# Kernel optimization log

Measured on AMD Instinct MI355X. Metric: run time of the kernel, lower is better.

Reference implementation:

```python
import jax, jax.numpy as jnp
import numpy as np

B, S, H, D = 2, 2048, 16, 64


def setup_inputs() -> dict:
    key = jax.random.key(0)
    kq, kk, kv, km = jax.random.split(key, 4)
    q = jax.random.normal(kq, (B, S, H, D), dtype=jnp.float32)
    k = jax.random.normal(kk, (B, S, H, D), dtype=jnp.float32)
    v = jax.random.normal(kv, (B, S, H, D), dtype=jnp.float32)
    pattern_mask = jax.random.bernoulli(km, 0.1, (S, S))
    return {"q": q, "k": k, "v": v, "pattern_mask": pattern_mask}


def reference(q, k, v, pattern_mask):
    # Faithful math of the torch module: for each query row i, attend only to
    # columns j where pattern_mask[i, j]; softmax over the selected columns
    # per (batch, head); rows with no selected columns produce zeros.
    head_dim = q.shape[-1]
    scale = 1.0 / jnp.sqrt(jnp.asarray(head_dim, dtype=q.dtype))
    # scores: [B, H, S_q, S_k]
    scores = jnp.einsum('bihd,bjhd->bhij', q, k) * scale
    neg = jnp.finfo(scores.dtype).min
    masked = jnp.where(pattern_mask[None, None, :, :], scores, neg)
    attn = jax.nn.softmax(masked, axis=-1)
    # zero out rows with no active columns (softmax over all-masked row is uniform garbage)
    row_has = jnp.any(pattern_mask, axis=-1)  # [S]
    attn = jnp.where(row_has[None, None, :, None], attn, jnp.zeros((), dtype=attn.dtype))
    # output: [B, S, H, D]
    out = jnp.einsum('bhij,bjhd->bihd', attn, v)
    return out
```

## Files before the change

kernel.cpp:

```cpp
#include <hip/hip_runtime.h>
#include <hip/hip_bf16.h>
#include <math.h>

#define SLEN 2048
#define NBATCH 2
#define NH 16
#define DH 64
#define WPR 64
#define NROUND 32
#define IMGB 8192
#define CONVBLK (NBATCH * NH * NROUND)
#define PACKBLK (SLEN * WPR / 256)

typedef __attribute__((ext_vector_type(4))) short short4v;
typedef __attribute__((ext_vector_type(8))) short short8v;
typedef __attribute__((ext_vector_type(4))) float float4v;
typedef __attribute__((ext_vector_type(16))) float float16v;

typedef __attribute__((address_space(1))) void gas_void;
typedef __attribute__((address_space(3))) void las_void;

__device__ __forceinline__ unsigned short f2bf(float f) {
  unsigned u = __float_as_uint(f);
  u += 0x7fffu + ((u >> 16) & 1u);
  return (unsigned short)(u >> 16);
}

__device__ __forceinline__ float fexp2(float x) {
#if __has_builtin(__builtin_amdgcn_exp2f)
  return __builtin_amdgcn_exp2f(x);
#else
  return __expf(x * 0.6931471805599453f);
#endif
}

__device__ __forceinline__ unsigned pack_bf2(float a, float b) {
  unsigned ua = __float_as_uint(a); ua += 0x7fffu + ((ua >> 16) & 1u);
  unsigned ub = __float_as_uint(b); ub += 0x7fffu + ((ub >> 16) & 1u);
  return __builtin_amdgcn_perm(ub, ua, 0x07060302u);
}

__device__ __forceinline__ unsigned cvtpk(float lo, float hi) {
  unsigned r;
  asm("v_cvt_pk_bf16_f32 %0, %1, %2" : "=v"(r) : "v"(lo), "v"(hi));
  return r;
}

__device__ __forceinline__ unsigned nib4(unsigned w) {
  return ((w * 0x01020408u) >> 24) & 0xFu;
}

__device__ __forceinline__ int vcol(int p) {
  const int kc = 2 * (p >> 5) + ((p >> 4) & 1);
  return 16 * kc + 8 * ((p >> 2) & 1) + 4 * ((p >> 3) & 1) + (p & 3);
}

__global__ __launch_bounds__(256) void prep_kernel(
    const float* __restrict__ kk, const float* __restrict__ vv,
    const void* __restrict__ mask,
    char* __restrict__ kb, char* __restrict__ vb,
    unsigned* __restrict__ packed) {
  const int tid = threadIdx.x;
  if (blockIdx.x >= CONVBLK) {
    const int w = (blockIdx.x - CONVBLK) * 256 + tid;
    const uint4* bp = (const uint4*)((const char*)mask + (size_t)w * 32);
    uint4 x = bp[0], y = bp[1];
    const unsigned orw = (x.x | x.y) | (x.z | x.w) | (y.x | y.y) | (y.z | y.w);
    __shared__ int s0, sm;
    if (tid == 0) { s0 = 0; sm = 0; }
    __syncthreads();
    const int lane0 = ((tid & 63) == 0);
    if (__any((orw & 0x000000ffu) != 0) && lane0) atomicOr(&s0, 1);
    if (__any((orw & 0xffffff00u) != 0) && lane0) atomicOr(&sm, 1);
    __syncthreads();
    unsigned bits;
    if (s0 && sm) {
      bits = nib4(x.x) | (nib4(x.y) << 4) | (nib4(x.z) << 8) | (nib4(x.w) << 12) |
             (nib4(y.x) << 16) | (nib4(y.y) << 20) | (nib4(y.z) << 24) | (nib4(y.w) << 28);
    } else {
      const unsigned* m = (const unsigned*)mask + (size_t)w * 32;
      bits = 0u;
#pragma unroll
      for (int j = 0; j < 32; j++) bits |= (m[j] ? 1u : 0u) << j;
    }
    packed[w] = bits;
    return;
  }
  const int bid = blockIdx.x;
  const int t = bid & 31;
  const int bh = bid >> 5;
  const int b = bh >> 4, h = bh & 15;
  char* kimg = kb + (size_t)bid * IMGB;
  char* vimg = vb + (size_t)bid * IMGB;

  {
    const int r = tid >> 2;
    const int dg = (tid & 3) << 4;
    const float* src = kk + (((size_t)(b * SLEN + t * 64 + r) * NH + h) * DH + dg);
    char* rowp = kimg + r * 128;
    const int swzk = (r & 7) << 4;
#pragma unroll
    for (int i = 0; i < 4; i++) {
      float4v x = *(const float4v*)(src + i * 4);
      const int d0 = dg + i * 4;
      const int off = (d0 * 2) ^ swzk;
      union { unsigned u[2]; short4v s4; } cv;
      cv.u[0] = pack_bf2(x.x, x.y);
      cv.u[1] = pack_bf2(x.z, x.w);
      *(short4v*)(rowp + off) = cv.s4;
    }
  }
  {
    const int d = tid >> 2;
    const int kg = (tid & 3) << 4;
    char* rowp = vimg + d * 128;
    const int swzv = (d & 7) << 4;
    const float* src = vv + ((size_t)(b * SLEN + t * 64 + kg) * NH + h) * DH + d;
#pragma unroll
    for (int i = 0; i < 16; i++) {
      const int p = kg + i;
      float x = src[(size_t)i * (NH * DH)];
      const int off = (vcol(p) * 2) ^ swzv;
      *(unsigned short*)(rowp + off) = f2bf(x);
    }
  }
}

__global__ __launch_bounds__(256, 2) void sattn_fast7(
    const float* __restrict__ q, const unsigned* __restrict__ pmask,
    const char* __restrict__ kb, const char* __restrict__ vb,
    float* __restrict__ out) {
  __shared__ __align__(16) char Kbuf[2][IMGB];
  __shared__ __align__(16) char Vbuf[2][IMGB];

  const int tid = threadIdx.x;
  const int xcd = blockIdx.x & 7;
  const int j = blockIdx.x >> 3;
  const int bh = xcd * 4 + (j >> 4);
  const int chunk = j & 15;
  const int b = bh >> 4;
  const int hd = bh & 15;
  const int wave = tid >> 6;
  const int lane = tid & 63;
  const int l31 = lane & 31;
  const int hl = lane >> 5;
  const int swz = (l31 & 7) << 4;

  const int qrow = chunk * 128 + wave * 32 + l31;
  const int qw = qrow * WPR;

  const float SCL2 = 0.18033688011112042f;
  short8v qf[4];
  {
    const float* qp = q + (((size_t)b * SLEN + qrow) * NH + hd) * DH;
#pragma unroll
    for (int ds = 0; ds < 4; ds++) {
      float4v x0 = *(const float4v*)(qp + ds * 16 + hl * 8);
      float4v x1 = *(const float4v*)(qp + ds * 16 + hl * 8 + 4);
      union { unsigned u[4]; short8v s8; } cv;
      cv.u[0] = pack_bf2(x0.x * SCL2, x0.y * SCL2);
      cv.u[1] = pack_bf2(x0.z * SCL2, x0.w * SCL2);
      cv.u[2] = pack_bf2(x1.x * SCL2, x1.y * SCL2);
      cv.u[3] = pack_bf2(x1.z * SCL2, x1.w * SCL2);
      qf[ds] = cv.s8;
    }
  }

  short8v ones;
#pragma unroll
  for (int i = 0; i < 8; i++) ones[i] = (short)0x3F80;

  const char* gK = kb + (size_t)bh * (NROUND * IMGB) + tid * 16;
  const char* gV = vb + (size_t)bh * (NROUND * IMGB) + tid * 16;

  float16v acc0 = {}, acc1 = {}, lacc = {};

  uint2 m = *(const uint2*)&pmask[qw];

  {
    char* lK = &Kbuf[0][0] + tid * 16;
    char* lV = &Vbuf[0][0] + tid * 16;
#pragma unroll
    for (int i = 0; i < 2; i++) {
      __builtin_amdgcn_global_load_lds((gas_void*)(gK + i * 4096), (las_void*)(lK + i * 4096), 16, 0, 0);
      __builtin_amdgcn_global_load_lds((gas_void*)(gV + i * 4096), (las_void*)(lV + i * 4096), 16, 0, 0);
    }
  }
  __syncthreads();

  for (int t = 0; t < NROUND; t++) {
    const int bt = t & 1;
    const unsigned m0 = m.x, m1 = m.y;
    if (t + 1 < NROUND) {
      m = *(const uint2*)&pmask[qw + 2 * (t + 1)];
      const char* nK = gK + (size_t)(t + 1) * IMGB;
      const char* nV = gV + (size_t)(t + 1) * IMGB;
      char* lK = &Kbuf[bt ^ 1][0] + tid * 16;
      char* lV = &Vbuf[bt ^ 1][0] + tid * 16;
#pragma unroll
      for (int i = 0; i < 2; i++) {
        __builtin_amdgcn_global_load_lds((gas_void*)(nK + i * 4096), (las_void*)(lK + i * 4096), 16, 0, 0);
        __builtin_amdgcn_global_load_lds((gas_void*)(nV + i * 4096), (las_void*)(lV + i * 4096), 16, 0, 0);
      }
    }

    const char* Kl = &Kbuf[bt][0];
    float16v st0, st1;
    __builtin_amdgcn_s_setprio(1);
    {
      float16v z = {};
#pragma unroll
      for (int ds = 0; ds < 4; ds++) {
        short8v kf = *(const short8v*)(Kl + (l31)*128 + ((ds * 32 + hl * 16) ^ swz));
        z = __builtin_amdgcn_mfma_f32_32x32x16_bf16(kf, qf[ds], z, 0, 0, 0);
      }
      st0 = z;
    }
    {
      float16v z = {};
#pragma unroll
      for (int ds = 0; ds < 4; ds++) {
        short8v kf = *(const short8v*)(Kl + (32 + l31) * 128 + ((ds * 32 + hl * 16) ^ swz));
        z = __builtin_amdgcn_mfma_f32_32x32x16_bf16(kf, qf[ds], z, 0, 0, 0);
      }
      st1 = z;
    }
    __builtin_amdgcn_s_setprio(0);

    float p0[16], p1[16];
#pragma unroll
    for (int u = 0; u < 4; u++) {
      const unsigned hw0 = m0 >> (8 * u + 4 * hl);
      const unsigned hw1 = m1 >> (8 * u + 4 * hl);
      {
        float a0 = fexp2(st0[4 * u + 0]); a0 = (hw0 & 1u) ? a0 : 0.f;
        float a1 = fexp2(st0[4 * u + 1]); a1 = (hw0 & 2u) ? a1 : 0.f;
        float a2 = fexp2(st0[4 * u + 2]); a2 = (hw0 & 4u) ? a2 : 0.f;
        float a3 = fexp2(st0[4 * u + 3]); a3 = (hw0 & 8u) ? a3 : 0.f;
        p0[4 * u + 0] = a0; p0[4 * u + 1] = a1; p0[4 * u + 2] = a2; p0[4 * u + 3] = a3;
      }
      {
        float a0 = fexp2(st1[4 * u + 0]); a0 = (hw1 & 1u) ? a0 : 0.f;
        float a1 = fexp2(st1[4 * u + 1]); a1 = (hw1 & 2u) ? a1 : 0.f;
        float a2 = fexp2(st1[4 * u + 2]); a2 = (hw1 & 4u) ? a2 : 0.f;
        float a3 = fexp2(st1[4 * u + 3]); a3 = (hw1 & 8u) ? a3 : 0.f;
        p1[4 * u + 0] = a0; p1[4 * u + 1] = a1; p1[4 * u + 2] = a2; p1[4 * u + 3] = a3;
      }
    }
    short8v pf[4];
    {
      union { unsigned u[4]; short8v s8; } c0, c1, c2, c3;
#pragma unroll
      for (int jj = 0; jj < 4; jj++) {
        c0.u[jj] = cvtpk(p0[2 * jj], p0[2 * jj + 1]);
        c1.u[jj] = cvtpk(p0[8 + 2 * jj], p0[8 + 2 * jj + 1]);
        c2.u[jj] = cvtpk(p1[2 * jj], p1[2 * jj + 1]);
        c3.u[jj] = cvtpk(p1[8 + 2 * jj], p1[8 + 2 * jj + 1]);
      }
      pf[0] = c0.s8; pf[1] = c1.s8; pf[2] = c2.s8; pf[3] = c3.s8;
    }

    const char* Vl = &Vbuf[bt][0];
    __builtin_amdgcn_s_setprio(1);
#pragma unroll
    for (int kc = 0; kc < 4; kc++) {
      short8v vf0 = *(const short8v*)(Vl + (l31)*128 + ((kc * 32 + hl * 16) ^ swz));
      acc0 = __builtin_amdgcn_mfma_f32_32x32x16_bf16(vf0, pf[kc], acc0, 0, 0, 0);
      short8v vf1 = *(const short8v*)(Vl + (32 + l31) * 128 + ((kc * 32 + hl * 16) ^ swz));
      acc1 = __builtin_amdgcn_mfma_f32_32x32x16_bf16(vf1, pf[kc], acc1, 0, 0, 0);
      lacc = __builtin_amdgcn_mfma_f32_32x32x16_bf16(ones, pf[kc], lacc, 0, 0, 0);
    }
    __builtin_amdgcn_s_setprio(0);
    __syncthreads();
  }

  const float l = lacc[0];
  const float inv = (l > 0.f) ? 1.f / l : 0.f;
  float* op = out + (((size_t)b * SLEN + qrow) * NH + hd) * DH;
#pragma unroll
  for (int u = 0; u < 4; u++) {
    float4v o0, o1;
    o0.x = acc0[4 * u + 0] * inv; o0.y = acc0[4 * u + 1] * inv;
    o0.z = acc0[4 * u + 2] * inv; o0.w = acc0[4 * u + 3] * inv;
    o1.x = acc1[4 * u + 0] * inv; o1.y = acc1[4 * u + 1] * inv;
    o1.z = acc1[4 * u + 2] * inv; o1.w = acc1[4 * u + 3] * inv;
    *(float4v*)(op + 8 * u + 4 * hl) = o0;
    *(float4v*)(op + 32 + 8 * u + 4 * hl) = o1;
  }
}

__global__ __launch_bounds__(256) void sattn_fallback(
    const float* __restrict__ q, const float* __restrict__ kk,
    const float* __restrict__ vv, const unsigned int* __restrict__ pmask,
    float* __restrict__ out) {
  __shared__ __align__(16) unsigned short Kt[16 * 64];
  __shared__ __align__(16) unsigned short Vt[64 * 20];

  const int tid = threadIdx.x;
  const int chunk = blockIdx.x & 31;
  const int bh = blockIdx.x >> 5;
  const int b = bh >> 4;
  const int h = bh & 15;
  const int wave = tid >> 6;
  const int lane = tid & 63;
  const int lq = lane & 15;
  const int g = lane >> 4;

  const int qrow = chunk * 64 + wave * 16 + lq;

  short4v qf[4];
  {
    const float* qp = q + (((size_t)b * SLEN + qrow) * NH + h) * DH;
#pragma unroll
    for (int ks = 0; ks < 4; ks++) {
      float4v x = *(const float4v*)(qp + ks * 16 + g * 4);
      short4v s;
      s.x = (short)f2bf(x.x); s.y = (short)f2bf(x.y);
      s.z = (short)f2bf(x.z); s.w = (short)f2bf(x.w);
      qf[ks] = s;
    }
  }

  const int srow = tid >> 4;
  const int scol = (tid & 15) * 4;
  const size_t kvbase = (size_t)b * SLEN * (NH * DH) + (size_t)h * DH;

  float4v acc[4] = {};
  float m_run = -INFINITY;
  float l_run = 0.f;

  for (int t = 0; t < SLEN / 16; t++) {
    const int kbase = t * 16;
    __syncthreads();
    {
      const size_t rowoff = kvbase + (size_t)(kbase + srow) * (NH * DH) + scol;
      float4v x = *(const float4v*)(kk + rowoff);
      short4v s;
      s.x = (short)f2bf(x.x); s.y = (short)f2bf(x.y);
      s.z = (short)f2bf(x.z); s.w = (short)f2bf(x.w);
      const int off = (scol * 2) ^ ((srow & 7) << 4);
      *(short4v*)((char*)Kt + srow * 128 + off) = s;

      float4v y = *(const float4v*)(vv + rowoff);
      Vt[(scol + 0) * 20 + srow] = f2bf(y.x);
      Vt[(scol + 1) * 20 + srow] = f2bf(y.y);
      Vt[(scol + 2) * 20 + srow] = f2bf(y.z);
      Vt[(scol + 3) * 20 + srow] = f2bf(y.w);
    }
    __syncthreads();

    float4v stv = {0.f, 0.f, 0.f, 0.f};
#pragma unroll
    for (int ks = 0; ks < 4; ks++) {
      const int off = ((ks * 16 + g * 4) * 2) ^ ((lq & 7) << 4);
      short4v kf = *(const short4v*)((const char*)Kt + lq * 128 + off);
      stv = __builtin_amdgcn_mfma_f32_16x16x16bf16_1k(kf, qf[ks], stv, 0, 0, 0);
    }

    const unsigned int mw = pmask[qrow * WPR + (kbase >> 5)];
    const int shift = (kbase & 16) + g * 4;
    float sc[4];
    float tmax = -INFINITY;
#pragma unroll
    for (int r = 0; r < 4; r++) {
      bool a = (mw >> (shift + r)) & 1u;
      sc[r] = a ? stv[r] * 0.125f : -INFINITY;
      tmax = fmaxf(tmax, sc[r]);
    }
    tmax = fmaxf(tmax, __shfl_xor(tmax, 16));
    tmax = fmaxf(tmax, __shfl_xor(tmax, 32));
    const float mnew = fmaxf(m_run, tmax);
    const float muse = (mnew > -1e37f) ? mnew : 0.f;
    const float alpha = __expf(m_run - muse);
    float p[4], tsum = 0.f;
#pragma unroll
    for (int r = 0; r < 4; r++) {
      p[r] = __expf(sc[r] - muse);
      tsum += p[r];
    }
    tsum += __shfl_xor(tsum, 16);
    tsum += __shfl_xor(tsum, 32);
    l_run = l_run * alpha + tsum;
    m_run = mnew;

    short4v pfv;
    pfv.x = (short)f2bf(p[0]); pfv.y = (short)f2bf(p[1]);
    pfv.z = (short)f2bf(p[2]); pfv.w = (short)f2bf(p[3]);

#pragma unroll
    for (int n = 0; n < 4; n++) {
      acc[n][0] *= alpha; acc[n][1] *= alpha;
      acc[n][2] *= alpha; acc[n][3] *= alpha;
      short4v vf = *(const short4v*)((const char*)Vt + ((n * 16 + lq) * 20 + g * 4) * 2);
      acc[n] = __builtin_amdgcn_mfma_f32_16x16x16bf16_1k(vf, pfv, acc[n], 0, 0, 0);
    }
  }

  const float inv = (l_run > 0.f) ? 1.f / l_run : 0.f;
  float* op = out + (((size_t)b * SLEN + qrow) * NH + h) * DH;
#pragma unroll
  for (int n = 0; n < 4; n++) {
    float4v o;
    o.x = acc[n][0] * inv; o.y = acc[n][1] * inv;
    o.z = acc[n][2] * inv; o.w = acc[n][3] * inv;
    *(float4v*)(op + n * 16 + g * 4) = o;
  }
}

extern "C" void kernel_launch(void* const* d_in, const int* in_sizes, int n_in,
                              void* d_out, int out_size, void* d_ws, size_t ws_size,
                              hipStream_t stream) {
  const float* q = (const float*)d_in[0];
  const float* k = (const float*)d_in[1];
  const float* v = (const float*)d_in[2];
  const void* mask = d_in[3];
  float* out = (float*)d_out;

  unsigned int* packed = (unsigned int*)((char*)d_ws + 256);
  char* kb = (char*)d_ws + (1 << 20);
  char* vb = kb + (size_t)NBATCH * NH * NROUND * IMGB;
  const size_t need = (size_t)(1 << 20) + 2 * (size_t)NBATCH * NH * NROUND * IMGB;

  prep_kernel<<<CONVBLK + PACKBLK, 256, 0, stream>>>(k, v, mask, kb, vb, packed);
  if (ws_size >= need) {
    sattn_fast7<<<NBATCH * NH * (SLEN / 128), 256, 0, stream>>>(q, packed, kb, vb, out);
  } else {
    sattn_fallback<<<NBATCH * NH * (SLEN / 64), 256, 0, stream>>>(q, k, v, packed, out);
  }
}
```

Measured before the change: 80.54 us.

## Load K/V MFMA fragments directly from global into registers, drop LDS staging

The prep kernel now writes K and V for each 64-key tile as a single 16KB image laid out in per-lane MFMA fragment order. The attention kernel then loads these fragments straight from global memory into registers, prefetching the next tile while computing the current one. This removes the LDS double buffer, the async global-to-LDS copies and the per-round __syncthreads. The row-sum MFMA against a ones vector is replaced by a scalar sum of the exp values plus one cross-half shuffle; the cost is more register pressure and every wave reading K/V from global or L2 separately.

New measurement: 69.59 us. 13.6% less time.

```diff
diff --git a/kernel.cpp b/kernel.cpp
--- a/kernel.cpp
+++ b/kernel.cpp
@@ -8,7 +8,7 @@
 #define DH 64
 #define WPR 64
 #define NROUND 32
-#define IMGB 8192
+#define TILEB 16384
 #define CONVBLK (NBATCH * NH * NROUND)
 #define PACKBLK (SLEN * WPR / 256)
 
@@ -16,9 +16,6 @@
 typedef __attribute__((ext_vector_type(8))) short short8v;
 typedef __attribute__((ext_vector_type(4))) float float4v;
 typedef __attribute__((ext_vector_type(16))) float float16v;
-
-typedef __attribute__((address_space(1))) void gas_void;
-typedef __attribute__((address_space(3))) void las_void;
 
 __device__ __forceinline__ unsigned short f2bf(float f) {
   unsigned u = __float_as_uint(f);
@@ -50,16 +47,10 @@
   return ((w * 0x01020408u) >> 24) & 0xFu;
 }
 
-__device__ __forceinline__ int vcol(int p) {
-  const int kc = 2 * (p >> 5) + ((p >> 4) & 1);
-  return 16 * kc + 8 * ((p >> 2) & 1) + 4 * ((p >> 3) & 1) + (p & 3);
-}
-
 __global__ __launch_bounds__(256) void prep_kernel(
     const float* __restrict__ kk, const float* __restrict__ vv,
     const void* __restrict__ mask,
-    char* __restrict__ kb, char* __restrict__ vb,
-    unsigned* __restrict__ packed) {
+    char* __restrict__ img, unsigned* __restrict__ packed) {
   const int tid = threadIdx.x;
   if (blockIdx.x >= CONVBLK) {
     const int w = (blockIdx.x - CONVBLK) * 256 + tid;
@@ -90,49 +81,47 @@
   const int t = bid & 31;
   const int bh = bid >> 5;
   const int b = bh >> 4, h = bh & 15;
-  char* kimg = kb + (size_t)bid * IMGB;
-  char* vimg = vb + (size_t)bid * IMGB;
+  char* timg = img + (size_t)bid * TILEB;
 
   {
     const int r = tid >> 2;
     const int dg = (tid & 3) << 4;
     const float* src = kk + (((size_t)(b * SLEN + t * 64 + r) * NH + h) * DH + dg);
-    char* rowp = kimg + r * 128;
-    const int swzk = (r & 7) << 4;
-#pragma unroll
-    for (int i = 0; i < 4; i++) {
-      float4v x = *(const float4v*)(src + i * 4);
-      const int d0 = dg + i * 4;
-      const int off = (d0 * 2) ^ swzk;
-      union { unsigned u[2]; short4v s4; } cv;
-      cv.u[0] = pack_bf2(x.x, x.y);
-      cv.u[1] = pack_bf2(x.z, x.w);
-      *(short4v*)(rowp + off) = cv.s4;
-    }
+    const int f = ((r >> 5) << 2) + (dg >> 4);
+    char* base = timg + f * 1024 + (r & 31) * 16;
+    float4v x0 = *(const float4v*)(src);
+    float4v x1 = *(const float4v*)(src + 4);
+    float4v x2 = *(const float4v*)(src + 8);
+    float4v x3 = *(const float4v*)(src + 12);
+    union { unsigned u[4]; short8v s8; } lo, hi;
+    lo.u[0] = pack_bf2(x0.x, x0.y); lo.u[1] = pack_bf2(x0.z, x0.w);
+    lo.u[2] = pack_bf2(x1.x, x1.y); lo.u[3] = pack_bf2(x1.z, x1.w);
+    hi.u[0] = pack_bf2(x2.x, x2.y); hi.u[1] = pack_bf2(x2.z, x2.w);
+    hi.u[2] = pack_bf2(x3.x, x3.y); hi.u[3] = pack_bf2(x3.z, x3.w);
+    *(short8v*)(base) = lo.s8;
+    *(short8v*)(base + 512) = hi.s8;
   }
   {
     const int d = tid >> 2;
     const int kg = (tid & 3) << 4;
-    char* rowp = vimg + d * 128;
-    const int swzv = (d & 7) << 4;
     const float* src = vv + ((size_t)(b * SLEN + t * 64 + kg) * NH + h) * DH + d;
+    const int fbase = 8 + ((d >> 5) << 2);
+    const int l31d = d & 31;
 #pragma unroll
     for (int i = 0; i < 16; i++) {
       const int p = kg + i;
       float x = src[(size_t)i * (NH * DH)];
-      const int off = (vcol(p) * 2) ^ swzv;
-      *(unsigned short*)(rowp + off) = f2bf(x);
-    }
-  }
-}
-
-__global__ __launch_bounds__(256, 2) void sattn_fast7(
+      const int f = fbase + 2 * (p >> 5) + ((p >> 4) & 1);
+      const int lane = ((p >> 2) & 1) * 32 + l31d;
+      const int slot = 4 * ((p >> 3) & 1) + (p & 3);
+      *(unsigned short*)(timg + f * 1024 + lane * 16 + slot * 2) = f2bf(x);
+    }
+  }
+}
+
+__global__ __launch_bounds__(256, 2) void sattn_fast8(
     const float* __restrict__ q, const unsigned* __restrict__ pmask,
-    const char* __restrict__ kb, const char* __restrict__ vb,
-    float* __restrict__ out) {
-  __shared__ __align__(16) char Kbuf[2][IMGB];
-  __shared__ __align__(16) char Vbuf[2][IMGB];
-
+    const char* __restrict__ img, float* __restrict__ out) {
   const int tid = threadIdx.x;
   const int xcd = blockIdx.x & 7;
   const int j = blockIdx.x >> 3;
@@ -144,7 +133,6 @@
   const int lane = tid & 63;
   const int l31 = lane & 31;
   const int hl = lane >> 5;
-  const int swz = (l31 & 7) << 4;
 
   const int qrow = chunk * 128 + wave * 32 + l31;
   const int qw = qrow * WPR;
@@ -166,66 +154,55 @@
     }
   }
 
-  short8v ones;
-#pragma unroll
-  for (int i = 0; i < 8; i++) ones[i] = (short)0x3F80;
-
-  const char* gK = kb + (size_t)bh * (NROUND * IMGB) + tid * 16;
-  const char* gV = vb + (size_t)bh * (NROUND * IMGB) + tid * 16;
-
-  float16v acc0 = {}, acc1 = {}, lacc = {};
-
+  const char* pt = img + (size_t)bh * (NROUND * TILEB) + lane * 16;
+
+  float16v acc0 = {}, acc1 = {};
+  float lsum = 0.f;
+
+  short8v kf0 = *(const short8v*)(pt + 0 * 1024);
+  short8v kf1 = *(const short8v*)(pt + 1 * 1024);
+  short8v kf2 = *(const short8v*)(pt + 2 * 1024);
+  short8v kf3 = *(const short8v*)(pt + 3 * 1024);
+  short8v kf4 = *(const short8v*)(pt + 4 * 1024);
+  short8v kf5 = *(const short8v*)(pt + 5 * 1024);
+  short8v kf6 = *(const short8v*)(pt + 6 * 1024);
+  short8v kf7 = *(const short8v*)(pt + 7 * 1024);
+  short8v vf0 = *(const short8v*)(pt + 8 * 1024);
+  short8v vf1 = *(const short8v*)(pt + 9 * 1024);
+  short8v vf2 = *(const short8v*)(pt + 10 * 1024);
+  short8v vf3 = *(const short8v*)(pt + 11 * 1024);
+  short8v vf4 = *(const short8v*)(pt + 12 * 1024);
+  short8v vf5 = *(const short8v*)(pt + 13 * 1024);
+  short8v vf6 = *(const short8v*)(pt + 14 * 1024);
+  short8v vf7 = *(const short8v*)(pt + 15 * 1024);
   uint2 m = *(const uint2*)&pmask[qw];
 
-  {
-    char* lK = &Kbuf[0][0] + tid * 16;
-    char* lV = &Vbuf[0][0] + tid * 16;
-#pragma unroll
-    for (int i = 0; i < 2; i++) {
-      __builtin_amdgcn_global_load_lds((gas_void*)(gK + i * 4096), (las_void*)(lK + i * 4096), 16, 0, 0);
-      __builtin_amdgcn_global_load_lds((gas_void*)(gV + i * 4096), (las_void*)(lV + i * 4096), 16, 0, 0);
-    }
-  }
-  __syncthreads();
-
   for (int t = 0; t < NROUND; t++) {
-    const int bt = t & 1;
     const unsigned m0 = m.x, m1 = m.y;
-    if (t + 1 < NROUND) {
-      m = *(const uint2*)&pmask[qw + 2 * (t + 1)];
-      const char* nK = gK + (size_t)(t + 1) * IMGB;
-      const char* nV = gV + (size_t)(t + 1) * IMGB;
-      char* lK = &Kbuf[bt ^ 1][0] + tid * 16;
-      char* lV = &Vbuf[bt ^ 1][0] + tid * 16;
-#pragma unroll
-      for (int i = 0; i < 2; i++) {
-        __builtin_amdgcn_global_load_lds((gas_void*)(nK + i * 4096), (las_void*)(lK + i * 4096), 16, 0, 0);
-        __builtin_amdgcn_global_load_lds((gas_void*)(nV + i * 4096), (las_void*)(lV + i * 4096), 16, 0, 0);
-      }
-    }
-
-    const char* Kl = &Kbuf[bt][0];
-    float16v st0, st1;
+    const int tn = (t + 1 < NROUND) ? t + 1 : t;
+    const char* pn = pt + (size_t)tn * TILEB;
+
     __builtin_amdgcn_s_setprio(1);
-    {
-      float16v z = {};
-#pragma unroll
-      for (int ds = 0; ds < 4; ds++) {
-        short8v kf = *(const short8v*)(Kl + (l31)*128 + ((ds * 32 + hl * 16) ^ swz));
-        z = __builtin_amdgcn_mfma_f32_32x32x16_bf16(kf, qf[ds], z, 0, 0, 0);
-      }
-      st0 = z;
-    }
-    {
-      float16v z = {};
-#pragma unroll
-      for (int ds = 0; ds < 4; ds++) {
-        short8v kf = *(const short8v*)(Kl + (32 + l31) * 128 + ((ds * 32 + hl * 16) ^ swz));
-        z = __builtin_amdgcn_mfma_f32_32x32x16_bf16(kf, qf[ds], z, 0, 0, 0);
-      }
-      st1 = z;
-    }
+    float16v st0 = {}, st1 = {};
+    st0 = __builtin_amdgcn_mfma_f32_32x32x16_bf16(kf0, qf[0], st0, 0, 0, 0);
+    st1 = __builtin_amdgcn_mfma_f32_32x32x16_bf16(kf4, qf[0], st1, 0, 0, 0);
+    st0 = __builtin_amdgcn_mfma_f32_32x32x16_bf16(kf1, qf[1], st0, 0, 0, 0);
+    st1 = __builtin_amdgcn_mfma_f32_32x32x16_bf16(kf5, qf[1], st1, 0, 0, 0);
+    st0 = __builtin_amdgcn_mfma_f32_32x32x16_bf16(kf2, qf[2], st0, 0, 0, 0);
+    st1 = __builtin_amdgcn_mfma_f32_32x32x16_bf16(kf6, qf[2], st1, 0, 0, 0);
+    st0 = __builtin_amdgcn_mfma_f32_32x32x16_bf16(kf3, qf[3], st0, 0, 0, 0);
+    st1 = __builtin_amdgcn_mfma_f32_32x32x16_bf16(kf7, qf[3], st1, 0, 0, 0);
     __builtin_amdgcn_s_setprio(0);
+
+    kf0 = *(const short8v*)(pn + 0 * 1024);
+    kf1 = *(const short8v*)(pn + 1 * 1024);
+    kf2 = *(const short8v*)(pn + 2 * 1024);
+    kf3 = *(const short8v*)(pn + 3 * 1024);
+    kf4 = *(const short8v*)(pn + 4 * 1024);
+    kf5 = *(const short8v*)(pn + 5 * 1024);
+    kf6 = *(const short8v*)(pn + 6 * 1024);
+    kf7 = *(const short8v*)(pn + 7 * 1024);
+    m = *(const uint2*)&pmask[qw + 2 * tn];
 
     float p0[16], p1[16];
 #pragma unroll
@@ -237,6 +214,7 @@
         float a1 = fexp2(st0[4 * u + 1]); a1 = (hw0 & 2u) ? a1 : 0.f;
         float a2 = fexp2(st0[4 * u + 2]); a2 = (hw0 & 4u) ? a2 : 0.f;
         float a3 = fexp2(st0[4 * u + 3]); a3 = (hw0 & 8u) ? a3 : 0.f;
+        lsum += (a0 + a1) + (a2 + a3);
         p0[4 * u + 0] = a0; p0[4 * u + 1] = a1; p0[4 * u + 2] = a2; p0[4 * u + 3] = a3;
       }
       {
@@ -244,10 +222,11 @@
         float a1 = fexp2(st1[4 * u + 1]); a1 = (hw1 & 2u) ? a1 : 0.f;
         float a2 = fexp2(st1[4 * u + 2]); a2 = (hw1 & 4u) ? a2 : 0.f;
         float a3 = fexp2(st1[4 * u + 3]); a3 = (hw1 & 8u) ? a3 : 0.f;
+        lsum += (a0 + a1) + (a2 + a3);
         p1[4 * u + 0] = a0; p1[4 * u + 1] = a1; p1[4 * u + 2] = a2; p1[4 * u + 3] = a3;
       }
     }
-    short8v pf[4];
+    short8v pf0, pf1, pf2, pf3;
     {
       union { unsigned u[4]; short8v s8; } c0, c1, c2, c3;
 #pragma unroll
@@ -257,25 +236,32 @@
         c2.u[jj] = cvtpk(p1[2 * jj], p1[2 * jj + 1]);
         c3.u[jj] = cvtpk(p1[8 + 2 * jj], p1[8 + 2 * jj + 1]);
       }
-      pf[0] = c0.s8; pf[1] = c1.s8; pf[2] = c2.s8; pf[3] = c3.s8;
-    }
-
-    const char* Vl = &Vbuf[bt][0];
+      pf0 = c0.s8; pf1 = c1.s8; pf2 = c2.s8; pf3 = c3.s8;
+    }
+
     __builtin_amdgcn_s_setprio(1);
-#pragma unroll
-    for (int kc = 0; kc < 4; kc++) {
-      short8v vf0 = *(const short8v*)(Vl + (l31)*128 + ((kc * 32 + hl * 16) ^ swz));
-      acc0 = __builtin_amdgcn_mfma_f32_32x32x16_bf16(vf0, pf[kc], acc0, 0, 0, 0);
-      short8v vf1 = *(const short8v*)(Vl + (32 + l31) * 128 + ((kc * 32 + hl * 16) ^ swz));
-      acc1 = __builtin_amdgcn_mfma_f32_32x32x16_bf16(vf1, pf[kc], acc1, 0, 0, 0);
-      lacc = __builtin_amdgcn_mfma_f32_32x32x16_bf16(ones, pf[kc], lacc, 0, 0, 0);
-    }
+    acc0 = __builtin_amdgcn_mfma_f32_32x32x16_bf16(vf0, pf0, acc0, 0, 0, 0);
+    acc1 = __builtin_amdgcn_mfma_f32_32x32x16_bf16(vf4, pf0, acc1, 0, 0, 0);
+    acc0 = __builtin_amdgcn_mfma_f32_32x32x16_bf16(vf1, pf1, acc0, 0, 0, 0);
+    acc1 = __builtin_amdgcn_mfma_f32_32x32x16_bf16(vf5, pf1, acc1, 0, 0, 0);
+    acc0 = __builtin_amdgcn_mfma_f32_32x32x16_bf16(vf2, pf2, acc0, 0, 0, 0);
+    acc1 = __builtin_amdgcn_mfma_f32_32x32x16_bf16(vf6, pf2, acc1, 0, 0, 0);
+    acc0 = __builtin_amdgcn_mfma_f32_32x32x16_bf16(vf3, pf3, acc0, 0, 0, 0);
+    acc1 = __builtin_amdgcn_mfma_f32_32x32x16_bf16(vf7, pf3, acc1, 0, 0, 0);
     __builtin_amdgcn_s_setprio(0);
-    __syncthreads();
-  }
-
-  const float l = lacc[0];
-  const float inv = (l > 0.f) ? 1.f / l : 0.f;
+
+    vf0 = *(const short8v*)(pn + 8 * 1024);
+    vf1 = *(const short8v*)(pn + 9 * 1024);
+    vf2 = *(const short8v*)(pn + 10 * 1024);
+    vf3 = *(const short8v*)(pn + 11 * 1024);
+    vf4 = *(const short8v*)(pn + 12 * 1024);
+    vf5 = *(const short8v*)(pn + 13 * 1024);
+    vf6 = *(const short8v*)(pn + 14 * 1024);
+    vf7 = *(const short8v*)(pn + 15 * 1024);
+  }
+
+  lsum += __shfl_xor(lsum, 32);
+  const float inv = (lsum > 0.f) ? 1.f / lsum : 0.f;
   float* op = out + (((size_t)b * SLEN + qrow) * NH + hd) * DH;
 #pragma unroll
   for (int u = 0; u < 4; u++) {
@@ -417,13 +403,12 @@
   float* out = (float*)d_out;
 
   unsigned int* packed = (unsigned int*)((char*)d_ws + 256);
-  char* kb = (char*)d_ws + (1 << 20);
-  char* vb = kb + (size_t)NBATCH * NH * NROUND * IMGB;
-  const size_t need = (size_t)(1 << 20) + 2 * (size_t)NBATCH * NH * NROUND * IMGB;
-
-  prep_kernel<<<CONVBLK + PACKBLK, 256, 0, stream>>>(k, v, mask, kb, vb, packed);
+  char* img = (char*)d_ws + (1 << 20);
+  const size_t need = (size_t)(1 << 20) + (size_t)CONVBLK * TILEB;
+
+  prep_kernel<<<CONVBLK + PACKBLK, 256, 0, stream>>>(k, v, mask, img, packed);
   if (ws_size >= need) {
-    sattn_fast7<<<NBATCH * NH * (SLEN / 128), 256, 0, stream>>>(q, packed, kb, vb, out);
+    sattn_fast8<<<NBATCH * NH * (SLEN / 128), 256, 0, stream>>>(q, packed, img, out);
   } else {
     sattn_fallback<<<NBATCH * NH * (SLEN / 64), 256, 0, stream>>>(q, k, v, packed, out);
   }
```
